# Kernel tuning notes

Hardware: AMD Instinct MI355X
Metric: run time of the kernel (lower is better)

Reference implementation:

```python
import jax, jax.numpy as jnp
import numpy as np

EPS = 1e-8
FS = 10000
WIN_LEN = 256          # N_FRAME
HOP = WIN_LEN // 2     # 128
NFFT = 2 * WIN_LEN     # 512
NUMBAND = 15
MINFREQ = 150
N_INTEL = 30           # N, number of frames per intelligibility segment
BETA = -15.0
DYN_RANGE = 40.0


def _thirdoct(fs, nfft, num_bands, min_freq):
    """One-third octave band matrix (pystoi.utils.thirdoct)."""
    f = np.linspace(0, fs, nfft + 1)[: nfft // 2 + 1]
    k = np.arange(num_bands, dtype=np.float64)
    freq_low = min_freq * np.power(2.0, (2 * k - 1) / 6)
    freq_high = min_freq * np.power(2.0, (2 * k + 1) / 6)
    obm = np.zeros((num_bands, len(f)), dtype=np.float32)
    for i in range(num_bands):
        fl = int(np.argmin(np.square(f - freq_low[i])))
        fh = int(np.argmin(np.square(f - freq_high[i])))
        obm[i, fl:fh] = 1.0
    return obm


def _frame(x, framelen, hop):
    """x: (B, T) -> (B, nf, framelen) sliding frames (static index gather)."""
    T = x.shape[-1]
    nf = (T - framelen) // hop + 1
    idx = np.arange(framelen)[None, :] + hop * np.arange(nf)[:, None]
    return x[:, idx]


def _stoi(est, tgt, win, obm):
    B = tgt.shape[0]
    # ---- VAD: remove silent frames (stable-partition kept frames to front) ----
    xf = _frame(tgt, WIN_LEN, HOP) * win           # (B, nf, L)
    yf = _frame(est, WIN_LEN, HOP) * win
    energies = 20.0 * jnp.log10(jnp.linalg.norm(xf, axis=-1) + EPS)  # (B, nf)
    mask = (energies.max(-1, keepdims=True) - DYN_RANGE - energies) < 0
    nf = xf.shape[1]
    # stable argsort: kept (mask=True -> key 0) frames first, original order preserved
    order = jnp.argsort(jnp.logical_not(mask).astype(jnp.int32), axis=-1)
    xf = jnp.take_along_axis(xf, order[..., None], axis=1)
    yf = jnp.take_along_axis(yf, order[..., None], axis=1)
    counts = mask.sum(-1)                          # (B,) number of kept frames
    keep = (jnp.arange(nf)[None, :] < counts[:, None]).astype(xf.dtype)
    xf = xf * keep[..., None]
    yf = yf * keep[..., None]

    # ---- overlap-and-add (framelen == 2 * hop) -> (B, (nf+1)*HOP) ----
    def ola(fr):
        a = fr[:, :, :HOP].reshape(B, -1)
        b = fr[:, :, HOP:].reshape(B, -1)
        return jnp.pad(a, ((0, 0), (0, HOP))) + jnp.pad(b, ((0, 0), (HOP, 0)))

    x_sil = ola(xf)
    y_sil = ola(yf)

    # mask sorted descending then first element dropped -> ones at positions < count-1
    m = (jnp.arange(nf - 1)[None, :] < (counts[:, None] - 1)).astype(xf.dtype)  # (B, nf-1)

    # ---- STFT via framing + rfft (last frame dropped, as in module) ----
    def stft(x):
        fr = _frame(x, WIN_LEN, HOP)[:, :-1] * win        # (B, nf-1, L)
        return jnp.fft.rfft(fr, n=NFFT, axis=-1)          # (B, nf-1, F)

    x_spec = stft(x_sil) * m[..., None]
    y_spec = stft(y_sil) * m[..., None]

    # ---- one-third octave band energies ----
    x_tob = jnp.sqrt(jnp.einsum('kf,bnf->bkn', obm, jnp.abs(x_spec) ** 2) + EPS)
    y_tob = jnp.sqrt(jnp.einsum('kf,bnf->bkn', obm, jnp.abs(y_spec) ** 2) + EPS)

    # ---- N_INTEL-frame segments (unfold) ----
    n_stft = x_tob.shape[-1]
    M = n_stft - N_INTEL + 1
    sidx = np.arange(N_INTEL)[:, None] + np.arange(M)[None, :]
    x_seg = x_tob[:, :, sidx]                      # (B, K, N, M)
    y_seg = y_tob[:, :, sidx]
    m2 = m[:, N_INTEL - 1:]                        # (B, M)
    x_seg = x_seg * m2[:, None, None, :]
    y_seg = y_seg * m2[:, None, None, :]

    # ---- clipped, normalized correlation (non-extended STOI) ----
    norm_const = jnp.linalg.norm(x_seg, axis=2, keepdims=True) / (
        jnp.linalg.norm(y_seg, axis=2, keepdims=True) + EPS)
    clip_val = 10.0 ** (-BETA / 20.0)
    y_prim = jnp.minimum(y_seg * norm_const, x_seg * (1.0 + clip_val))
    y_prim = y_prim - y_prim.mean(2, keepdims=True)
    x_c = x_seg - x_seg.mean(2, keepdims=True)
    y_prim = y_prim / (jnp.linalg.norm(y_prim, axis=2, keepdims=True) + EPS)
    x_c = x_c / (jnp.linalg.norm(x_c, axis=2, keepdims=True) + EPS)
    corr = (y_prim * x_c).sum(2).mean(1)           # (B, M)
    out = corr.sum(-1) / (m2.sum(-1) + EPS)        # (B,)
    return -out


def setup_inputs() -> dict:
    key = jax.random.key(0)
    k1, k2 = jax.random.split(key)
    B, T = 32, 320000
    targets = jax.random.normal(k1, (B, T), dtype=jnp.float32)
    est_targets = targets + 0.3 * jax.random.normal(k2, (B, T), dtype=jnp.float32)
    win = jnp.asarray(np.hanning(WIN_LEN + 2)[1:-1], dtype=jnp.float32)
    obm = jnp.asarray(_thirdoct(FS, NFFT, NUMBAND, MINFREQ))
    return {"est_targets": est_targets, "targets": targets, "win": win, "obm": obm}


def reference(est_targets, targets, win, obm):
    return _stoi(est_targets, targets, win, obm)
```

## Files before the change

kernel.cpp:

```cpp
#include <hip/hip_runtime.h>
#include <math.h>

#define EPSF 1e-8f
#define WIN_LEN 256
#define HOP 128
#define NBINS 257
#define NUMBAND 15
#define NFRAMES 2499
#define NSTFT 2498
#define N_INTEL 30
#define NSEG 2469
#define NB 32
#define T_LEN 320000
#define CLIP_VAL 5.623413251903491f
#define NHALF 2500
#define AB_STRIDE 2560
#define NWX 1249

typedef float v2f __attribute__((ext_vector_type(2)));
typedef float v4f __attribute__((ext_vector_type(4)));

__device__ __forceinline__ void pk_fma_blo(v2f& d, v2f a, v2f b) {
    asm("v_pk_fma_f32 %0, %1, %2, %0 op_sel:[0,0,0] op_sel_hi:[1,0,1]"
        : "+v"(d) : "v"(a), "v"(b));
}
__device__ __forceinline__ void pk_fma_rot(v2f& d, v2f a, v2f b) {
    asm("v_pk_fma_f32 %0, %1, %2, %0 op_sel:[1,1,0] op_sel_hi:[0,1,1] neg_lo:[1,0,0]"
        : "+v"(d) : "v"(a), "v"(b));
}
__device__ __forceinline__ void pk_fma_nbhi(v2f& d, v2f a, v2f b) {
    asm("v_pk_fma_f32 %0, %1, %2, %0 op_sel:[0,1,0] op_sel_hi:[1,1,1] neg_lo:[1,0,0] neg_hi:[1,0,0]"
        : "+v"(d) : "v"(a), "v"(b));
}
__device__ __forceinline__ void pk_fma_s(v2f& d, v2f a, float s) {
    const v2f bv = { s, s };
    asm("v_pk_fma_f32 %0, %1, %2, %0"
        : "+v"(d) : "v"(a), "v"(bv));
}
__device__ __forceinline__ v2f pk_mul_blo(v2f a, v2f b) {
    v2f d;
    asm("v_pk_mul_f32 %0, %1, %2 op_sel:[0,0] op_sel_hi:[1,0]"
        : "=v"(d) : "v"(a), "v"(b));
    return d;
}
__device__ __forceinline__ v2f pk_mul_bhi(v2f a, v2f b) {
    v2f d;
    asm("v_pk_mul_f32 %0, %1, %2 op_sel:[0,1] op_sel_hi:[1,1]"
        : "=v"(d) : "v"(a), "v"(b));
    return d;
}
__device__ __forceinline__ v2f pk_mul_s(v2f a, float s) {
    const v2f bv = { s, s };
    v2f d;
    asm("v_pk_mul_f32 %0, %1, %2" : "=v"(d) : "v"(a), "v"(bv));
    return d;
}
__device__ __forceinline__ v2f pk_add(v2f a, v2f b) {
    v2f d;
    asm("v_pk_add_f32 %0, %1, %2" : "=v"(d) : "v"(a), "v"(b));
    return d;
}
__device__ __forceinline__ v2f pk_sub(v2f a, v2f b) {
    v2f d;
    asm("v_pk_add_f32 %0, %1, %2 neg_lo:[0,1] neg_hi:[0,1]" : "=v"(d) : "v"(a), "v"(b));
    return d;
}
__device__ __forceinline__ v2f pk_bmi(v2f B, v2f D) {
    v2f d;
    asm("v_pk_add_f32 %0, %1, %2 op_sel:[1,0] op_sel_hi:[0,1] neg_hi:[1,0]"
        : "=v"(d) : "v"(D), "v"(B));
    return d;
}
__device__ __forceinline__ v2f pk_bpi(v2f B, v2f D) {
    v2f d;
    asm("v_pk_add_f32 %0, %1, %2 op_sel:[1,0] op_sel_hi:[0,1] neg_lo:[1,0]"
        : "=v"(d) : "v"(D), "v"(B));
    return d;
}
__device__ __forceinline__ v2f pk_cmul(v2f a, v2f b) {
    v2f t;
    asm("v_pk_mul_f32 %0, %1, %2 op_sel:[0,0] op_sel_hi:[1,0]"
        : "=v"(t) : "v"(a), "v"(b));
    asm("v_pk_fma_f32 %0, %1, %2, %0 op_sel:[1,1,0] op_sel_hi:[0,1,1] neg_lo:[1,0,0]"
        : "+v"(t) : "v"(a), "v"(b));
    return t;
}
__device__ __forceinline__ void pk_rot(v2f& cs, v2f cksk) {
    v2f t;
    asm("v_pk_mul_f32 %0, %1, %2 op_sel:[0,0] op_sel_hi:[1,0]"
        : "=v"(t) : "v"(cs), "v"(cksk));
    asm("v_pk_fma_f32 %0, %0, %1, %2 op_sel:[1,1,0] op_sel_hi:[0,1,1] neg_lo:[1,0,0]"
        : "+v"(cs) : "v"(cksk), "v"(t));
}
__device__ __forceinline__ void pk_cfma(v2f& acc, v2f g, float wr, float wi) {
    const v2f wv = { wr, wi };
    pk_fma_blo(acc, g, wv);
    pk_fma_rot(acc, g, wv);
}
__device__ __forceinline__ unsigned pk_f16(float a, float b) {
    unsigned u;
    asm("v_cvt_pkrtz_f16_f32 %0, %1, %2" : "=v"(u) : "v"(a), "v"(b));
    return u;
}
__device__ __forceinline__ v2f unpk_f16(unsigned u) {
    float lo, hi;
    asm("v_cvt_f32_f16 %0, %1" : "=v"(lo) : "v"(u));
    asm("v_lshrrev_b32 %0, 16, %1\n\tv_cvt_f32_f16 %0, %0" : "=v"(hi) : "v"(u));
    return (v2f){ lo, hi };
}

#define WS_COUNTS   0
#define WS_BANDLO   512
#define WS_BANDHI   768
#define WS_SRCFRM   5632
#define WS_XTOB     325632
#define WS_YTOB     5121792

__global__ __launch_bounds__(256)
void k1a_ab(const float* __restrict__ tgt, const float* __restrict__ win,
            const float* __restrict__ obm, float2* __restrict__ ab,
            int* __restrict__ band_lo, int* __restrict__ band_hi,
            float* __restrict__ out_)
{
    const int b = blockIdx.x;
    const int tid = threadIdx.x;
    const int h = blockIdx.y * 256 + tid;
    if (h < NHALF) {
        const float* xp = tgt + (size_t)b * T_LEN + (size_t)h * HOP;
        float sa = 0.f, sb = 0.f;
        #pragma unroll 4
        for (int u = 0; u < HOP; u += 4) {
            const float4 xv = *(const float4*)(xp + u);
            const float4 wl = *(const float4*)(win + u);
            const float4 wh = *(const float4*)(win + HOP + u);
            float a;
            a = xv.x * wl.x; sa = fmaf(a, a, sa);
            a = xv.y * wl.y; sa = fmaf(a, a, sa);
            a = xv.z * wl.z; sa = fmaf(a, a, sa);
            a = xv.w * wl.w; sa = fmaf(a, a, sa);
            a = xv.x * wh.x; sb = fmaf(a, a, sb);
            a = xv.y * wh.y; sb = fmaf(a, a, sb);
            a = xv.z * wh.z; sb = fmaf(a, a, sb);
            a = xv.w * wh.w; sb = fmaf(a, a, sb);
        }
        ab[(size_t)b * AB_STRIDE + h] = make_float2(sa, sb);
    }

    if (b == 0 && blockIdx.y == 0) {
        if (tid < NUMBAND) {
            int lo = -1, hi = 0;
            for (int k = 0; k < NBINS; ++k) {
                if (obm[tid * NBINS + k] != 0.f) { if (lo < 0) lo = k; hi = k + 1; }
            }
            band_lo[tid] = (lo < 0) ? 0 : lo;
            band_hi[tid] = hi;
        }
        __syncthreads();
        if (tid == 0) {
            int lo = NBINS, hi = 0;
            for (int i = 0; i < NUMBAND; ++i) {
                if (band_lo[i] < lo) lo = band_lo[i];
                if (band_hi[i] > hi) hi = band_hi[i];
            }
            band_lo[NUMBAND] = lo;
            band_hi[NUMBAND] = hi;
        }
        if (tid < NB) out_[tid] = 0.f;
    }
}

__global__ __launch_bounds__(256)
void k1b_scan(const float2* __restrict__ ab,
              int* __restrict__ counts, int* __restrict__ srcfrm)
{
    const int b = blockIdx.x;
    const int tid = threadIdx.x;
    __shared__ float nr[NFRAMES];
    __shared__ float red[256];
    __shared__ int   sc[256];

    const float2* abp = ab + (size_t)b * AB_STRIDE;
    for (int f = tid; f < NFRAMES; f += 256) {
        const float2 p0 = abp[f];
        const float2 p1 = abp[f + 1];
        nr[f] = sqrtf(p0.x + p1.y);
    }
    __syncthreads();

    float mx = 0.f;
    for (int f = tid; f < NFRAMES; f += 256) mx = fmaxf(mx, nr[f]);
    red[tid] = mx;
    __syncthreads();
    for (int s = 128; s > 0; s >>= 1) {
        if (tid < s) red[tid] = fmaxf(red[tid], red[tid + s]);
        __syncthreads();
    }
    const float thr = (red[0] + EPSF) * 0.01f;

    const int c0 = tid * 10;
    const int c1 = (c0 + 10 < NFRAMES) ? c0 + 10 : NFRAMES;
    int lc = 0;
    for (int f = c0; f < c1; ++f) if (nr[f] + EPSF > thr) ++lc;
    sc[tid] = lc;
    __syncthreads();
    #pragma unroll
    for (int off = 1; off < 256; off <<= 1) {
        int u = (tid >= off) ? sc[tid - off] : 0;
        __syncthreads();
        sc[tid] += u;
        __syncthreads();
    }
    if (tid == 0) counts[b] = sc[255];
    int pos = sc[tid] - lc;
    int* sf = srcfrm + b * NFRAMES;
    for (int f = c0; f < c1; ++f) if (nr[f] + EPSF > thr) sf[pos++] = f;
}

__global__ __launch_bounds__(128)
void k2_stft_tob(const float* __restrict__ est, const float* __restrict__ tgt,
                 const float* __restrict__ win,
                 const int* __restrict__ counts, const int* __restrict__ srcfrm,
                 const int* __restrict__ band_lo, const int* __restrict__ band_hi,
                 float* __restrict__ xtob, float* __restrict__ ytob)
{
    const int lin = blockIdx.x;
    const int xcd = lin & 7, cidx = lin >> 3;
    const int q = NWX >> 3, r = NWX & 7;
    const int rl = (xcd < r ? xcd * (q + 1) : r * (q + 1) + (xcd - r) * q) + cidx;

    const int wave = threadIdx.x >> 6;
    const int tid = threadIdx.x & 63;
    const int j = rl * 2 + wave;

    const int b = blockIdx.y;
    const int cntb = counts[b];
    const bool valid = (j < cntb - 1);

    __shared__ float    frf[2][512];
    __shared__ unsigned sxh[2][2][16][34];

    const int* sf = srcfrm + b * NFRAMES;
    const float* xg = tgt + (size_t)b * T_LEN;
    const float* yg = est + (size_t)b * T_LEN;

    {
        const int t4 = 4 * tid;
        v4f xv = { 0.f, 0.f, 0.f, 0.f }, yv = xv;
        const v4f wa = *(const v4f*)&win[t4];
        if (valid) {
            const int k0 = sf[j];
            if (tid < 32) {
                xv = *(const v4f*)&xg[k0 * HOP + t4] * wa;
                yv = *(const v4f*)&yg[k0 * HOP + t4] * wa;
                if (j >= 1) {
                    const int km = sf[j - 1];
                    const v4f wb = *(const v4f*)&win[HOP + t4];
                    xv += *(const v4f*)&xg[km * HOP + HOP + t4] * wb;
                    yv += *(const v4f*)&yg[km * HOP + HOP + t4] * wb;
                }
            } else {
                const int kp = sf[j + 1];
                const v4f wb = *(const v4f*)&win[t4 - HOP];
                xv = *(const v4f*)&xg[k0 * HOP + t4] * wa
                   + *(const v4f*)&xg[kp * HOP + t4 - HOP] * wb;
                yv = *(const v4f*)&yg[k0 * HOP + t4] * wa
                   + *(const v4f*)&yg[kp * HOP + t4 - HOP] * wb;
            }
        }
        xv *= wa; yv *= wa;
        const v4f lo = { xv.x, yv.x, xv.y, yv.y };
        const v4f hi = { xv.z, yv.z, xv.w, yv.w };
        *(v4f*)&frf[wave][2 * t4]     = lo;
        *(v4f*)&frf[wave][2 * t4 + 4] = hi;
    }
    __syncthreads();

    {
        const int m = tid & 3;
        const int c = tid >> 2;
        const float ke = (m == 0) ? 1.f : (m == 2) ? -1.f : 0.f;
        const float ki = (m == 1) ? -1.f : (m == 3) ? 1.f : 0.f;
        const float ang = -0.19634954084936207f * (float)m;
        const v2f cksk = { __cosf(ang), __sinf(ang) };
        v2f cs = { 1.f, 0.f };
        v2f URe[8], UIm[8];
        #pragma unroll
        for (int rr = 0; rr < 8; ++rr) {
            const v2f za = *(const v2f*)&frf[wave][2 * (16 * rr + c)];
            const v2f zb = *(const v2f*)&frf[wave][2 * (16 * rr + 128 + c)];
            v2f pre_re = za; pk_fma_s(pre_re, zb, ke);
            const v2f pre_im = pk_mul_s(zb, ki);
            v2f ur = pk_mul_blo(pre_re, cs); pk_fma_nbhi(ur, pre_im, cs);
            v2f ui = pk_mul_bhi(pre_re, cs); pk_fma_blo(ui, pre_im, cs);
            URe[rr] = ur; UIm[rr] = ui;
            pk_rot(cs, cksk);
        }
        v2f ARe[8], AIm[8];
        {
            const float C2 = 0.70710678118654752f;
            v2f dR, dI;
            #pragma unroll
            for (int rr = 0; rr < 4; ++rr) {
                ARe[rr] = pk_add(URe[rr], URe[rr + 4]);
                AIm[rr] = pk_add(UIm[rr], UIm[rr + 4]);
            }
            ARe[4] = pk_sub(URe[0], URe[4]);     AIm[4] = pk_sub(UIm[0], UIm[4]);
            dR = pk_sub(URe[1], URe[5]); dI = pk_sub(UIm[1], UIm[5]);
            ARe[5] = pk_mul_s(pk_add(dR, dI), C2);
            AIm[5] = pk_mul_s(pk_sub(dI, dR), C2);
            dR = pk_sub(URe[2], URe[6]); dI = pk_sub(UIm[2], UIm[6]);
            ARe[6] = dI;                         AIm[6] = pk_mul_s(dR, -1.f);
            dR = pk_sub(URe[3], URe[7]); dI = pk_sub(UIm[3], UIm[7]);
            ARe[7] = pk_mul_s(pk_sub(dI, dR), C2);
            AIm[7] = pk_mul_s(pk_add(dR, dI), -C2);
        }
        v2f BRe[8], BIm[8];
        #pragma unroll
        for (int g = 0; g < 8; g += 4) {
            BRe[g + 0] = pk_add(ARe[g + 0], ARe[g + 2]);  BIm[g + 0] = pk_add(AIm[g + 0], AIm[g + 2]);
            BRe[g + 1] = pk_add(ARe[g + 1], ARe[g + 3]);  BIm[g + 1] = pk_add(AIm[g + 1], AIm[g + 3]);
            BRe[g + 2] = pk_sub(ARe[g + 0], ARe[g + 2]);  BIm[g + 2] = pk_sub(AIm[g + 0], AIm[g + 2]);
            const v2f dR = pk_sub(ARe[g + 1], ARe[g + 3]);
            const v2f dI = pk_sub(AIm[g + 1], AIm[g + 3]);
            BRe[g + 3] = dI;  BIm[g + 3] = pk_mul_s(dR, -1.f);
        }
        const int kmap[8] = { 0, 4, 2, 6, 1, 5, 3, 7 };
        #pragma unroll
        for (int p = 0; p < 8; ++p) {
            const int pb = p & ~1;
            v2f oR, oI;
            if (p & 1) { oR = pk_sub(BRe[pb], BRe[pb + 1]); oI = pk_sub(BIm[pb], BIm[pb + 1]); }
            else       { oR = pk_add(BRe[pb], BRe[pb + 1]); oI = pk_add(BIm[pb], BIm[pb + 1]); }
            const int mj = m + 4 * kmap[p];
            sxh[wave][0][c][mj] = pk_f16(oR.x, oI.x);
            sxh[wave][1][c][mj] = pk_f16(oR.y, oI.y);
        }
    }
    __syncthreads();

    const int blo = band_lo[NUMBAND];
    const int base = blo & ~31;
    float* px = frf[wave];
    float* py = frf[wave] + 224;
    {
        const int m2 = tid & 31;
        const int sig = tid >> 5;
        const float ang = -0.012271846303085130f * (float)(base + m2);
        const v2f cksk = { __cosf(ang), __sinf(ang) };
        v2f cs = { 1.f, 0.f };
        v2f V[16];
        #pragma unroll
        for (int t0 = 0; t0 < 16; ++t0) {
            const v2f s = unpk_f16(sxh[wave][sig][t0][m2]);
            V[t0] = (t0 == 0) ? s : pk_cmul(cs, s);
            pk_rot(cs, cksk);
        }
        v2f G[4][4];
        #pragma unroll
        for (int rr = 0; rr < 4; ++rr) {
            const v2f A = pk_add(V[rr], V[rr + 8]);
            const v2f B = pk_sub(V[rr], V[rr + 8]);
            const v2f C = pk_add(V[rr + 4], V[rr + 12]);
            const v2f D = pk_sub(V[rr + 4], V[rr + 12]);
            G[0][rr] = pk_add(A, C);
            G[2][rr] = pk_sub(A, C);
            G[1][rr] = pk_bmi(B, D);
            G[3][rr] = pk_bpi(B, D);
        }
        float* pout = sig ? py : px;
        #define C1 0.92387953251f
        #define S1 0.38268343236f
        #define C2c 0.70710678119f
        {
            const v2f a_ = pk_add(pk_add(G[0][0], G[0][1]), pk_add(G[0][2], G[0][3]));
            pout[0 * 32 + m2] = fmaf(a_.x, a_.x, a_.y * a_.y);
        }
        #define XOUT(P, D, W1R, W1I, W2R, W2I, W3R, W3I) { \
            v2f a_ = G[D][0]; \
            pk_cfma(a_, G[D][1], W1R, W1I); \
            pk_cfma(a_, G[D][2], W2R, W2I); \
            pk_cfma(a_, G[D][3], W3R, W3I); \
            pout[(P) * 32 + m2] = fmaf(a_.x, a_.x, a_.y * a_.y); }
        XOUT(1, 1,  C1, -S1,     C2c, -C2c,   S1, -C1)
        XOUT(2, 2,  C2c, -C2c,   0.f, -1.f,  -C2c, -C2c)
        XOUT(3, 3,  S1, -C1,    -C2c, -C2c,  -C1,  S1)
        {
            const v2f t1_ = pk_sub(G[0][0], G[0][2]);
            const v2f t2_ = pk_sub(G[0][1], G[0][3]);
            const v2f a_ = pk_bmi(t1_, t2_);
            pout[4 * 32 + m2] = fmaf(a_.x, a_.x, a_.y * a_.y);
        }
        XOUT(5, 1, -S1, -C1,    -C2c,  C2c,   C1,  S1)
        XOUT(6, 2, -C2c, -C2c,   0.f,  1.f,   C2c, -C2c)
        #undef XOUT
    }
    __syncthreads();

    if (tid < 4 * NUMBAND && valid) {
        const int band = tid >> 2, s = tid & 3;
        const int lop = band_lo[band] - base, hip = band_hi[band] - base;
        const int u0 = lop >> 1, ul = (hip - 1) >> 1;
        float sx = 0.f, sy = 0.f;
        for (int u = u0 + s; u <= ul; u += 4) {
            const v2f pvx = *(const v2f*)&px[2 * u];
            const v2f pvy = *(const v2f*)&py[2 * u];
            const float m0 = (2 * u >= lop) ? 1.f : 0.f;
            const float m1 = (2 * u + 1 < hip) ? 1.f : 0.f;
            sx = fmaf(m0, pvx.x, sx); sx = fmaf(m1, pvx.y, sx);
            sy = fmaf(m0, pvy.x, sy); sy = fmaf(m1, pvy.y, sy);
        }
        sx += __shfl_xor(sx, 1, 64);  sx += __shfl_xor(sx, 2, 64);
        sy += __shfl_xor(sy, 1, 64);  sy += __shfl_xor(sy, 2, 64);
        if (s == 0) {
            xtob[((size_t)b * NUMBAND + band) * NSTFT + j] = sqrtf(sx + EPSF);
            ytob[((size_t)b * NUMBAND + band) * NSTFT + j] = sqrtf(sy + EPSF);
        }
    }
}

__global__ __launch_bounds__(256)
void k3_corr(const float* __restrict__ xtob, const float* __restrict__ ytob,
             const int* __restrict__ counts, float* __restrict__ out_)
{
    const int bb = blockIdx.y;
    const int b = bb / NUMBAND;
    const int band = bb % NUMBAND;
    const int s_base = blockIdx.x * 256;
    const int tid = threadIdx.x;
    const int seg = s_base + tid;

    __shared__ v2f lxy[256 + N_INTEL - 1];
    const float* xr = xtob + ((size_t)b * NUMBAND + band) * NSTFT;
    const float* yr = ytob + ((size_t)b * NUMBAND + band) * NSTFT;
    for (int i = tid; i < 256 + N_INTEL - 1; i += 256) {
        const int g = s_base + i;
        v2f v = { 0.f, 0.f };
        if (g < NSTFT) v = (v2f){ xr[g], yr[g] };
        lxy[i] = v;
    }
    __syncthreads();

    int nvalid = counts[b] - N_INTEL;
    if (nvalid < 0) nvalid = 0;
    if (nvalid > NSEG) nvalid = NSEG;

    float d = 0.f;
    if (seg < nvalid) {
        float xv[N_INTEL], yv[N_INTEL];
        float sx2 = 0.f, sy2 = 0.f;
        #pragma unroll
        for (int i = 0; i < N_INTEL; ++i) {
            const v2f v = lxy[tid + i];
            xv[i] = v.x; yv[i] = v.y;
            sx2 = fmaf(xv[i], xv[i], sx2);
            sy2 = fmaf(yv[i], yv[i], sy2);
        }
        const float nc = sqrtf(sx2) / (sqrtf(sy2) + EPSF);
        float sy = 0.f, sx = 0.f;
        #pragma unroll
        for (int i = 0; i < N_INTEL; ++i) {
            const float yp = fminf(yv[i] * nc, xv[i] * (1.f + CLIP_VAL));
            yv[i] = yp;
            sy += yp; sx += xv[i];
        }
        const float my = sy * (1.f / N_INTEL);
        const float mxm = sx * (1.f / N_INTEL);
        float num = 0.f, dy = 0.f, dx2 = 0.f;
        #pragma unroll
        for (int i = 0; i < N_INTEL; ++i) {
            const float a = yv[i] - my;
            const float c = xv[i] - mxm;
            num = fmaf(a, c, num);
            dy  = fmaf(a, a, dy);
            dx2 = fmaf(c, c, dx2);
        }
        d = num / ((sqrtf(dy) + EPSF) * (sqrtf(dx2) + EPSF));
    }

    #pragma unroll
    for (int o = 32; o > 0; o >>= 1) d += __shfl_down(d, o, 64);
    __shared__ float wsum[4];
    const int lane = threadIdx.x & 63, wid = threadIdx.x >> 6;
    if (lane == 0) wsum[wid] = d;
    __syncthreads();
    if (threadIdx.x == 0) {
        const float scale = -1.f / ((float)NUMBAND * ((float)nvalid + EPSF));
        atomicAdd(&out_[b], (wsum[0] + wsum[1] + wsum[2] + wsum[3]) * scale);
    }
}

extern "C" void kernel_launch(void* const* d_in, const int* in_sizes, int n_in,
                              void* d_out, int out_size, void* d_ws, size_t ws_size,
                              hipStream_t stream) {
    (void)in_sizes; (void)n_in; (void)out_size; (void)ws_size;
    const float* est = (const float*)d_in[0];
    const float* tgt = (const float*)d_in[1];
    const float* win = (const float*)d_in[2];
    const float* obm = (const float*)d_in[3];
    float* out = (float*)d_out;

    char* ws = (char*)d_ws;
    int*   counts  = (int*)(ws + WS_COUNTS);
    int*   band_lo = (int*)(ws + WS_BANDLO);
    int*   band_hi = (int*)(ws + WS_BANDHI);
    int*   srcfrm  = (int*)(ws + WS_SRCFRM);
    float* xtob    = (float*)(ws + WS_XTOB);
    float* ytob    = (float*)(ws + WS_YTOB);
    float2* ab     = (float2*)xtob;

    k1a_ab<<<dim3(NB, 10), dim3(256), 0, stream>>>(tgt, win, obm, ab,
                                                   band_lo, band_hi, out);
    k1b_scan<<<dim3(NB), dim3(256), 0, stream>>>(ab, counts, srcfrm);
    k2_stft_tob<<<dim3(NWX, NB), dim3(128), 0, stream>>>(est, tgt, win, counts, srcfrm,
                                                         band_lo, band_hi, xtob, ytob);
    k3_corr<<<dim3((NSEG + 255) / 256, NB * NUMBAND), dim3(256), 0, stream>>>(xtob, ytob,
                                                                              counts, out);
}
```

Baseline: 173.0 us.

## Use packed complex FFT with conjugate-symmetry separation of x and y spectra

Changes the STFT stage from two separate real-channel FFT paths to a single complex FFT where x and y are packed as real and imaginary parts. Twiddles move into the first stage and the intermediate is kept as fp32 complex in shared memory instead of fp16. The spectra are split using Z[k] and Z[N-k] symmetry during the band sum, with the output stored as fp16. This should cut the packed-math instruction count and the twiddle rotation in the second stage. The cost is more shared-memory traffic for the fp32 intermediate and some fp16 rounding on the final spectrum.

```diff
diff --git a/kernel.cpp b/kernel.cpp
--- a/kernel.cpp
+++ b/kernel.cpp
@@ -28,26 +28,10 @@
     asm("v_pk_fma_f32 %0, %1, %2, %0 op_sel:[1,1,0] op_sel_hi:[0,1,1] neg_lo:[1,0,0]"
         : "+v"(d) : "v"(a), "v"(b));
 }
-__device__ __forceinline__ void pk_fma_nbhi(v2f& d, v2f a, v2f b) {
-    asm("v_pk_fma_f32 %0, %1, %2, %0 op_sel:[0,1,0] op_sel_hi:[1,1,1] neg_lo:[1,0,0] neg_hi:[1,0,0]"
-        : "+v"(d) : "v"(a), "v"(b));
-}
 __device__ __forceinline__ void pk_fma_s(v2f& d, v2f a, float s) {
     const v2f bv = { s, s };
     asm("v_pk_fma_f32 %0, %1, %2, %0"
         : "+v"(d) : "v"(a), "v"(bv));
-}
-__device__ __forceinline__ v2f pk_mul_blo(v2f a, v2f b) {
-    v2f d;
-    asm("v_pk_mul_f32 %0, %1, %2 op_sel:[0,0] op_sel_hi:[1,0]"
-        : "=v"(d) : "v"(a), "v"(b));
-    return d;
-}
-__device__ __forceinline__ v2f pk_mul_bhi(v2f a, v2f b) {
-    v2f d;
-    asm("v_pk_mul_f32 %0, %1, %2 op_sel:[0,1] op_sel_hi:[1,1]"
-        : "=v"(d) : "v"(a), "v"(b));
-    return d;
 }
 __device__ __forceinline__ v2f pk_mul_s(v2f a, float s) {
     const v2f bv = { s, s };
@@ -236,8 +220,8 @@
     const int cntb = counts[b];
     const bool valid = (j < cntb - 1);
 
-    __shared__ float    frf[2][512];
-    __shared__ unsigned sxh[2][2][16][34];
+    __shared__ float frf[2][512];
+    __shared__ v2f   sxr[2][16][34];
 
     const int* sf = srcfrm + b * NFRAMES;
     const float* xg = tgt + (size_t)b * T_LEN;
@@ -280,81 +264,69 @@
         const int c = tid >> 2;
         const float ke = (m == 0) ? 1.f : (m == 2) ? -1.f : 0.f;
         const float ki = (m == 1) ? -1.f : (m == 3) ? 1.f : 0.f;
-        const float ang = -0.19634954084936207f * (float)m;
-        const v2f cksk = { __cosf(ang), __sinf(ang) };
+        const float angm = -0.19634954084936207f * (float)m;
+        const v2f cksk = { __cosf(angm), __sinf(angm) };
+        const v2f zv = { 0.f, 0.f };
         v2f cs = { 1.f, 0.f };
-        v2f URe[8], UIm[8];
+        v2f U[8];
         #pragma unroll
         for (int rr = 0; rr < 8; ++rr) {
             const v2f za = *(const v2f*)&frf[wave][2 * (16 * rr + c)];
             const v2f zb = *(const v2f*)&frf[wave][2 * (16 * rr + 128 + c)];
-            v2f pre_re = za; pk_fma_s(pre_re, zb, ke);
-            const v2f pre_im = pk_mul_s(zb, ki);
-            v2f ur = pk_mul_blo(pre_re, cs); pk_fma_nbhi(ur, pre_im, cs);
-            v2f ui = pk_mul_bhi(pre_re, cs); pk_fma_blo(ui, pre_im, cs);
-            URe[rr] = ur; UIm[rr] = ui;
+            const v2f tb = pk_bmi(zv, zb);
+            v2f pre = za;
+            pk_fma_s(pre, zb, ke);
+            pk_fma_s(pre, tb, -ki);
+            U[rr] = pk_cmul(cs, pre);
             pk_rot(cs, cksk);
         }
-        v2f ARe[8], AIm[8];
+        const float C2 = 0.70710678118654752f;
+        v2f A[8];
+        A[0] = pk_add(U[0], U[4]); A[1] = pk_add(U[1], U[5]);
+        A[2] = pk_add(U[2], U[6]); A[3] = pk_add(U[3], U[7]);
         {
-            const float C2 = 0.70710678118654752f;
-            v2f dR, dI;
-            #pragma unroll
-            for (int rr = 0; rr < 4; ++rr) {
-                ARe[rr] = pk_add(URe[rr], URe[rr + 4]);
-                AIm[rr] = pk_add(UIm[rr], UIm[rr + 4]);
-            }
-            ARe[4] = pk_sub(URe[0], URe[4]);     AIm[4] = pk_sub(UIm[0], UIm[4]);
-            dR = pk_sub(URe[1], URe[5]); dI = pk_sub(UIm[1], UIm[5]);
-            ARe[5] = pk_mul_s(pk_add(dR, dI), C2);
-            AIm[5] = pk_mul_s(pk_sub(dI, dR), C2);
-            dR = pk_sub(URe[2], URe[6]); dI = pk_sub(UIm[2], UIm[6]);
-            ARe[6] = dI;                         AIm[6] = pk_mul_s(dR, -1.f);
-            dR = pk_sub(URe[3], URe[7]); dI = pk_sub(UIm[3], UIm[7]);
-            ARe[7] = pk_mul_s(pk_sub(dI, dR), C2);
-            AIm[7] = pk_mul_s(pk_add(dR, dI), -C2);
-        }
-        v2f BRe[8], BIm[8];
+            v2f d;
+            d = pk_sub(U[0], U[4]); A[4] = d;
+            d = pk_sub(U[1], U[5]); A[5] = pk_mul_s(pk_bmi(d, d), C2);
+            d = pk_sub(U[2], U[6]); A[6] = pk_bmi(zv, d);
+            d = pk_sub(U[3], U[7]); A[7] = pk_mul_s(pk_bmi(zv, pk_bmi(d, d)), C2);
+        }
+        v2f Bv[8];
         #pragma unroll
         for (int g = 0; g < 8; g += 4) {
-            BRe[g + 0] = pk_add(ARe[g + 0], ARe[g + 2]);  BIm[g + 0] = pk_add(AIm[g + 0], AIm[g + 2]);
-            BRe[g + 1] = pk_add(ARe[g + 1], ARe[g + 3]);  BIm[g + 1] = pk_add(AIm[g + 1], AIm[g + 3]);
-            BRe[g + 2] = pk_sub(ARe[g + 0], ARe[g + 2]);  BIm[g + 2] = pk_sub(AIm[g + 0], AIm[g + 2]);
-            const v2f dR = pk_sub(ARe[g + 1], ARe[g + 3]);
-            const v2f dI = pk_sub(AIm[g + 1], AIm[g + 3]);
-            BRe[g + 3] = dI;  BIm[g + 3] = pk_mul_s(dR, -1.f);
-        }
+            Bv[g + 0] = pk_add(A[g + 0], A[g + 2]);
+            Bv[g + 1] = pk_add(A[g + 1], A[g + 3]);
+            Bv[g + 2] = pk_sub(A[g + 0], A[g + 2]);
+            Bv[g + 3] = pk_bmi(zv, pk_sub(A[g + 1], A[g + 3]));
+        }
+        const float a0  = -0.012271846303085130f * (float)(m * c);
+        const float asr = -0.049087385212340517f * (float)c;
+        v2f bt = { __cosf(a0), __sinf(a0) };
+        const v2f stp = { __cosf(asr), __sinf(asr) };
+        v2f twj[8];
+        #pragma unroll
+        for (int jj = 0; jj < 8; ++jj) { twj[jj] = bt; pk_rot(bt, stp); }
         const int kmap[8] = { 0, 4, 2, 6, 1, 5, 3, 7 };
         #pragma unroll
         for (int p = 0; p < 8; ++p) {
             const int pb = p & ~1;
-            v2f oR, oI;
-            if (p & 1) { oR = pk_sub(BRe[pb], BRe[pb + 1]); oI = pk_sub(BIm[pb], BIm[pb + 1]); }
-            else       { oR = pk_add(BRe[pb], BRe[pb + 1]); oI = pk_add(BIm[pb], BIm[pb + 1]); }
-            const int mj = m + 4 * kmap[p];
-            sxh[wave][0][c][mj] = pk_f16(oR.x, oI.x);
-            sxh[wave][1][c][mj] = pk_f16(oR.y, oI.y);
+            const v2f o = (p & 1) ? pk_sub(Bv[pb], Bv[pb + 1])
+                                  : pk_add(Bv[pb], Bv[pb + 1]);
+            const int jj = kmap[p];
+            sxr[wave][c][m + 4 * jj] = pk_cmul(twj[jj], o);
         }
     }
     __syncthreads();
 
     const int blo = band_lo[NUMBAND];
     const int base = blo & ~31;
-    float* px = frf[wave];
-    float* py = frf[wave] + 224;
+    unsigned* zOut = (unsigned*)&frf[wave][0];
     {
         const int m2 = tid & 31;
-        const int sig = tid >> 5;
-        const float ang = -0.012271846303085130f * (float)(base + m2);
-        const v2f cksk = { __cosf(ang), __sinf(ang) };
-        v2f cs = { 1.f, 0.f };
+        const int half = tid >> 5;
         v2f V[16];
         #pragma unroll
-        for (int t0 = 0; t0 < 16; ++t0) {
-            const v2f s = unpk_f16(sxh[wave][sig][t0][m2]);
-            V[t0] = (t0 == 0) ? s : pk_cmul(cs, s);
-            pk_rot(cs, cksk);
-        }
+        for (int t0 = 0; t0 < 16; ++t0) V[t0] = sxr[wave][t0][m2];
         v2f G[4][4];
         #pragma unroll
         for (int rr = 0; rr < 4; ++rr) {
@@ -367,53 +339,61 @@
             G[1][rr] = pk_bmi(B, D);
             G[3][rr] = pk_bpi(B, D);
         }
-        float* pout = sig ? py : px;
         #define C1 0.92387953251f
         #define S1 0.38268343236f
         #define C2c 0.70710678119f
-        {
-            const v2f a_ = pk_add(pk_add(G[0][0], G[0][1]), pk_add(G[0][2], G[0][3]));
-            pout[0 * 32 + m2] = fmaf(a_.x, a_.x, a_.y * a_.y);
-        }
-        #define XOUT(P, D, W1R, W1I, W2R, W2I, W3R, W3I) { \
+        #define XOUTZ(SLOT, D, W1R, W1I, W2R, W2I, W3R, W3I) { \
             v2f a_ = G[D][0]; \
             pk_cfma(a_, G[D][1], W1R, W1I); \
             pk_cfma(a_, G[D][2], W2R, W2I); \
             pk_cfma(a_, G[D][3], W3R, W3I); \
-            pout[(P) * 32 + m2] = fmaf(a_.x, a_.x, a_.y * a_.y); }
-        XOUT(1, 1,  C1, -S1,     C2c, -C2c,   S1, -C1)
-        XOUT(2, 2,  C2c, -C2c,   0.f, -1.f,  -C2c, -C2c)
-        XOUT(3, 3,  S1, -C1,    -C2c, -C2c,  -C1,  S1)
-        {
-            const v2f t1_ = pk_sub(G[0][0], G[0][2]);
-            const v2f t2_ = pk_sub(G[0][1], G[0][3]);
-            const v2f a_ = pk_bmi(t1_, t2_);
-            pout[4 * 32 + m2] = fmaf(a_.x, a_.x, a_.y * a_.y);
-        }
-        XOUT(5, 1, -S1, -C1,    -C2c,  C2c,   C1,  S1)
-        XOUT(6, 2, -C2c, -C2c,   0.f,  1.f,   C2c, -C2c)
-        #undef XOUT
+            zOut[SLOT] = pk_f16(a_.x, a_.y); }
+        if (half == 0) {
+            { const v2f a_ = pk_add(pk_add(G[0][0], G[0][1]), pk_add(G[0][2], G[0][3]));
+              zOut[m2] = pk_f16(a_.x, a_.y); }
+            XOUTZ(m2 + 32, 1,  C1, -S1,     C2c, -C2c,   S1, -C1)
+            XOUTZ(m2 + 64, 2,  C2c, -C2c,   0.f, -1.f,  -C2c, -C2c)
+            XOUTZ(m2 + 96, 3,  S1, -C1,    -C2c, -C2c,  -C1,  S1)
+            { const v2f t1_ = pk_sub(G[0][0], G[0][2]);
+              const v2f t2_ = pk_sub(G[0][1], G[0][3]);
+              const v2f a_ = pk_bmi(t1_, t2_);
+              zOut[m2 + 128] = pk_f16(a_.x, a_.y); }
+            XOUTZ(m2 + 160, 1, -S1, -C1,    -C2c,  C2c,   C1,  S1)
+            XOUTZ(m2 + 192, 2, -C2c, -C2c,   0.f,  1.f,   C2c, -C2c)
+        } else {
+            XOUTZ(224 + m2,       1, -C1,  S1,    C2c, -C2c,  -S1,  C1)
+            XOUTZ(224 + m2 + 32,  2, -C2c,  C2c,  0.f, -1.f,   C2c,  C2c)
+            XOUTZ(224 + m2 + 64,  3, -S1,  C1,   -C2c, -C2c,   C1, -S1)
+            { const v2f t1_ = pk_sub(G[0][0], G[0][2]);
+              const v2f t2_ = pk_sub(G[0][1], G[0][3]);
+              const v2f a_ = pk_bpi(t1_, t2_);
+              zOut[224 + m2 + 96] = pk_f16(a_.x, a_.y); }
+            XOUTZ(224 + m2 + 128, 1,  S1,  C1,   -C2c,  C2c,  -C1, -S1)
+            XOUTZ(224 + m2 + 160, 2,  C2c,  C2c,  0.f,  1.f,  -C2c,  C2c)
+            XOUTZ(224 + m2 + 192, 3,  C1,  S1,    C2c,  C2c,   S1,  C1)
+        }
+        #undef XOUTZ
     }
     __syncthreads();
 
     if (tid < 4 * NUMBAND && valid) {
         const int band = tid >> 2, s = tid & 3;
-        const int lop = band_lo[band] - base, hip = band_hi[band] - base;
-        const int u0 = lop >> 1, ul = (hip - 1) >> 1;
+        const int lo = band_lo[band], hi = band_hi[band];
         float sx = 0.f, sy = 0.f;
-        for (int u = u0 + s; u <= ul; u += 4) {
-            const v2f pvx = *(const v2f*)&px[2 * u];
-            const v2f pvy = *(const v2f*)&py[2 * u];
-            const float m0 = (2 * u >= lop) ? 1.f : 0.f;
-            const float m1 = (2 * u + 1 < hip) ? 1.f : 0.f;
-            sx = fmaf(m0, pvx.x, sx); sx = fmaf(m1, pvx.y, sx);
-            sy = fmaf(m0, pvy.x, sy); sy = fmaf(m1, pvy.y, sy);
+        for (int k = lo + s; k < hi; k += 4) {
+            const int kk = k - base;
+            const v2f zk = unpk_f16(zOut[kk]);
+            const v2f zr = unpk_f16(zOut[448 - kk]);
+            const float e1 = zk.x + zr.x, e2 = zk.y - zr.y;
+            const float e3 = zk.y + zr.y, e4 = zk.x - zr.x;
+            sx = fmaf(e1, e1, sx); sx = fmaf(e2, e2, sx);
+            sy = fmaf(e3, e3, sy); sy = fmaf(e4, e4, sy);
         }
         sx += __shfl_xor(sx, 1, 64);  sx += __shfl_xor(sx, 2, 64);
         sy += __shfl_xor(sy, 1, 64);  sy += __shfl_xor(sy, 2, 64);
         if (s == 0) {
-            xtob[((size_t)b * NUMBAND + band) * NSTFT + j] = sqrtf(sx + EPSF);
-            ytob[((size_t)b * NUMBAND + band) * NSTFT + j] = sqrtf(sy + EPSF);
+            xtob[((size_t)b * NUMBAND + band) * NSTFT + j] = sqrtf(0.25f * sx + EPSF);
+            ytob[((size_t)b * NUMBAND + band) * NSTFT + j] = sqrtf(0.25f * sy + EPSF);
         }
     }
 }
```

Result: slower. 180.6 us (+4.4%).
